# Kernel optimization log

Measured on AMD Instinct MI355X. Metric: run time of the kernel, lower is better.

Reference implementation:

```python
import jax, jax.numpy as jnp
import numpy as np

N_NODES = 50000
N_EDGES = 1600000
F_IN = 128
HID = 128
N_CLS = 16


def setup_inputs() -> dict:
    key = jax.random.key(0)
    ks = jax.random.split(key, 8)
    x = jax.random.normal(ks[0], (N_NODES, F_IN), dtype=jnp.float32)
    edge_index = jax.random.randint(ks[1], (2, N_EDGES), 0, N_NODES, dtype=jnp.int64)
    W1 = jax.random.normal(ks[2], (F_IN, HID), dtype=jnp.float32) * (1.0 / np.sqrt(F_IN))
    b1 = jnp.zeros((HID,), dtype=jnp.float32)
    W2 = jax.random.normal(ks[3], (HID, HID), dtype=jnp.float32) * (1.0 / np.sqrt(HID))
    b2 = jnp.zeros((HID,), dtype=jnp.float32)
    W3 = jax.random.normal(ks[4], (HID, N_CLS), dtype=jnp.float32) * (1.0 / np.sqrt(HID))
    b3 = jnp.zeros((N_CLS,), dtype=jnp.float32)
    return {"x": x, "edge_index": edge_index, "W1": W1, "b1": b1,
            "W2": W2, "b2": b2, "W3": W3, "b3": b3}


def _gcn_norm(edge_index, n_nodes, dtype):
    # PyG gcn_norm with add_self_loops=True, improved=False
    loops = jnp.arange(n_nodes, dtype=edge_index.dtype)
    row = jnp.concatenate([edge_index[0], loops])  # source j
    col = jnp.concatenate([edge_index[1], loops])  # target i
    deg = jax.ops.segment_sum(jnp.ones(row.shape[0], dtype=dtype), col,
                              num_segments=n_nodes)
    dinv = jnp.where(deg > 0, jax.lax.rsqrt(deg), 0.0)
    norm = dinv[row] * dinv[col]  # [E + N]
    return row, col, norm


def _gcn_conv(h, W, b, row, col, norm, n_nodes):
    h = h @ W                              # [N, out] linear first (PyG order)
    msg = h[row] * norm[:, None]           # gather + per-edge scale
    agg = jax.ops.segment_sum(msg, col, num_segments=n_nodes)  # scatter-add
    return agg + b


def reference(x, edge_index, W1, b1, W2, b2, W3, b3):
    n = x.shape[0]
    row, col, norm = _gcn_norm(edge_index, n, x.dtype)
    h = jax.nn.relu(_gcn_conv(x, W1, b1, row, col, norm, n))
    h = jax.nn.relu(_gcn_conv(h, W2, b2, row, col, norm, n))
    h = jax.nn.relu(_gcn_conv(h, W3, b3, row, col, norm, n))
    return h
```

## Files before the change

### kernel.cpp

```cpp
#include <hip/hip_runtime.h>
#include <hip/hip_fp16.h>


static inline int cdiv(int a, int b) { return (a + b - 1) / b; }

__global__ __launch_bounds__(256) void k_zero_int(int* p, int n) {
    int i = blockIdx.x * 256 + threadIdx.x;
    if (i < n) p[i] = 0;
}

__global__ __launch_bounds__(256) void k_count(const int* __restrict__ col, int* cnt, int e) {
    int i = blockIdx.x * 256 + threadIdx.x;
    if (i < e) atomicAdd(&cnt[col[i]], 1);
}

__global__ __launch_bounds__(256) void k_scanA(const int* __restrict__ cnt, int* bsum,
                                               float* __restrict__ dinv, int n) {
    __shared__ int s[256];
    int t = threadIdx.x;
    int i = blockIdx.x * 256 + t;
    int v = (i < n) ? cnt[i] : 0;
    if (i < n) dinv[i] = rsqrtf((float)(v + 1));
    s[t] = v;
    __syncthreads();
    for (int off = 128; off > 0; off >>= 1) {
        if (t < off) s[t] += s[t + off];
        __syncthreads();
    }
    if (t == 0) bsum[blockIdx.x] = s[0];
}

__global__ __launch_bounds__(256) void k_scanB(int* bsum, int nb) {
    __shared__ int s[256];
    int t = threadIdx.x;
    int v = (t < nb) ? bsum[t] : 0;
    s[t] = v;
    for (int off = 1; off < 256; off <<= 1) {
        __syncthreads();
        int x = (t >= off) ? s[t - off] : 0;
        __syncthreads();
        s[t] += x;
    }
    __syncthreads();
    if (t < nb) bsum[t] = s[t] - v;
}

__global__ __launch_bounds__(256) void k_scanC(const int* __restrict__ cnt, const int* __restrict__ bsum,
                                               int* offs, int* cur, int n) {
    __shared__ int s[256];
    int t = threadIdx.x;
    int i = blockIdx.x * 256 + t;
    int v = (i < n) ? cnt[i] : 0;
    s[t] = v;
    for (int off = 1; off < 256; off <<= 1) {
        __syncthreads();
        int x = (t >= off) ? s[t - off] : 0;
        __syncthreads();
        s[t] += x;
    }
    __syncthreads();
    int ov = bsum[blockIdx.x] + s[t] - v;
    if (i <= n) offs[i] = ov;
    if (i < n) cur[i] = ov;
}

__global__ __launch_bounds__(256) void k_fill_xcd(const int* __restrict__ row, const int* __restrict__ col,
                                                  int* cur, unsigned short* __restrict__ csr,
                                                  int e, int n, int nblk) {
    int g = blockIdx.x & 7;
    int b = blockIdx.x >> 3;
    int rs = (n + 7) >> 3;
    int lo = g * rs;
    int hi = min(lo + rs, n);
    int stride = nblk * 256;
    for (int i = b * 256 + threadIdx.x; i < e; i += stride) {
        int c = col[i];
        if (c >= lo && c < hi) {
            int pos = atomicAdd(&cur[c], 1);
            csr[pos] = (unsigned short)row[i];
        }
    }
}

__global__ __launch_bounds__(256) void k_gemm128(const float* __restrict__ X, const float* __restrict__ W,
                                                 const float* __restrict__ dinv,
                                                 __half* __restrict__ Ah, int n) {
    __shared__ float sW[16][128];
    __shared__ float sX[16][128];
    int tid = threadIdx.x;

    int row0 = blockIdx.x * 128;
    int tx = tid & 15, ty = tid >> 4;
    float acc[8][8];
    #pragma unroll
    for (int i = 0; i < 8; ++i)
        #pragma unroll
        for (int j = 0; j < 8; ++j) acc[i][j] = 0.f;

    for (int k0 = 0; k0 < 128; k0 += 16) {
        __syncthreads();
        #pragma unroll
        for (int i = tid; i < 512; i += 256) {
            int kk = i >> 5, c4 = i & 31;
            *(float4*)&sW[kk][c4 * 4] = ((const float4*)W)[(size_t)(k0 + kk) * 32 + c4];
        }
        #pragma unroll
        for (int i = tid; i < 512; i += 256) {
            int r = i >> 2, kq = i & 3;
            int gr = row0 + r;
            float4 v = (gr < n) ? ((const float4*)X)[(size_t)gr * 32 + (k0 >> 2) + kq]
                                : make_float4(0.f, 0.f, 0.f, 0.f);
            sX[kq * 4 + 0][r] = v.x;
            sX[kq * 4 + 1][r] = v.y;
            sX[kq * 4 + 2][r] = v.z;
            sX[kq * 4 + 3][r] = v.w;
        }
        __syncthreads();
        #pragma unroll
        for (int kk = 0; kk < 16; ++kk) {
            float a[8], b[8];
            *(float4*)&a[0] = *(const float4*)&sX[kk][ty * 8];
            *(float4*)&a[4] = *(const float4*)&sX[kk][ty * 8 + 4];
            *(float4*)&b[0] = *(const float4*)&sW[kk][tx * 8];
            *(float4*)&b[4] = *(const float4*)&sW[kk][tx * 8 + 4];
            #pragma unroll
            for (int i = 0; i < 8; ++i)
                #pragma unroll
                for (int j = 0; j < 8; ++j)
                    acc[i][j] = fmaf(a[i], b[j], acc[i][j]);
        }
    }
    #pragma unroll
    for (int i = 0; i < 8; ++i) {
        int gr = row0 + ty * 8 + i;
        if (gr < n) {
            float di = dinv[gr];
            union { uint4 u; __half2 h[4]; } pk;
            pk.h[0] = __floats2half2_rn(di * acc[i][0], di * acc[i][1]);
            pk.h[1] = __floats2half2_rn(di * acc[i][2], di * acc[i][3]);
            pk.h[2] = __floats2half2_rn(di * acc[i][4], di * acc[i][5]);
            pk.h[3] = __floats2half2_rn(di * acc[i][6], di * acc[i][7]);
            ((uint4*)Ah)[(size_t)gr * 16 + tx] = pk.u;
        }
    }
}

__global__ __launch_bounds__(256) void k_gemm16(const float* __restrict__ X, const float* __restrict__ W,
                                                const float* __restrict__ dinv,
                                                __half* __restrict__ Ch, int n) {
    __shared__ float sX[16 * 132];
    __shared__ float sW[128 * 16];
    int tid = threadIdx.x;
    for (int i = tid; i < 512; i += 256)
        ((float4*)sW)[i] = ((const float4*)W)[i];
    int row0 = blockIdx.x * 16;
    for (int i = tid; i < 512; i += 256) {
        int r = i >> 5, c = i & 31;
        int gr = row0 + r;
        float4 v = (gr < n) ? ((const float4*)X)[(size_t)gr * 32 + c]
                            : make_float4(0.f, 0.f, 0.f, 0.f);
        *(float4*)&sX[r * 132 + c * 4] = v;
    }
    __syncthreads();

    int rl = tid >> 4, cj = tid & 15;
    float acc = 0.f;
    #pragma unroll 8
    for (int k = 0; k < 128; ++k)
        acc = fmaf(sX[rl * 132 + k], sW[k * 16 + cj], acc);
    int gr = row0 + rl;
    if (gr < n) Ch[(size_t)gr * 16 + cj] = __float2half_rn(dinv[gr] * acc);
}

__global__ __launch_bounds__(256) void k_agg128(const __half* __restrict__ Hh, const unsigned short* __restrict__ csr,
                                                const int* __restrict__ offs, const float* __restrict__ dinv,
                                                const float* __restrict__ b, float* __restrict__ out, int n) {
    int node = (blockIdx.x * 256 + threadIdx.x) >> 6;
    if (node >= n) return;
    int lane = threadIdx.x & 63;
    int sub  = lane & 31;
    int half = lane >> 5;
    const uint2* H2 = (const uint2*)Hh;
    int ed = offs[node], end = offs[node + 1];
    float4 acc = make_float4(0.f, 0.f, 0.f, 0.f);

    #define EDGE_ADD(R)                                                          \
        {                                                                        \
            uint2 q = H2[(size_t)(R) * 32 + sub];                                \
            float2 f01 = __half22float2(*(const __half2*)&q.x);                  \
            float2 f23 = __half22float2(*(const __half2*)&q.y);                  \
            acc.x += f01.x; acc.y += f01.y;                                      \
            acc.z += f23.x; acc.w += f23.y;                                      \
        }

    for (; ed + 7 < end; ed += 8) {
        int r0 = csr[ed     + half];
        int r1 = csr[ed + 2 + half];
        int r2 = csr[ed + 4 + half];
        int r3 = csr[ed + 6 + half];
        EDGE_ADD(r0); EDGE_ADD(r1); EDGE_ADD(r2); EDGE_ADD(r3);
    }
    #pragma unroll
    for (int s = 0; s < 4; ++s) {
        int idx = ed + 2 * s + half;
        if (idx < end) {
            int r = csr[idx];
            EDGE_ADD(r);
        }
    }
    #undef EDGE_ADD

    acc.x += __shfl_xor(acc.x, 32);
    acc.y += __shfl_xor(acc.y, 32);
    acc.z += __shfl_xor(acc.z, 32);
    acc.w += __shfl_xor(acc.w, 32);

    float di = dinv[node];
    uint2 qh = H2[(size_t)node * 32 + sub];
    float2 h01 = __half22float2(*(const __half2*)&qh.x);
    float2 h23 = __half22float2(*(const __half2*)&qh.y);
    float4 bv = ((const float4*)b)[sub];
    float4 o;
    o.x = fmaxf(fmaf(di, acc.x + h01.x, bv.x), 0.f);
    o.y = fmaxf(fmaf(di, acc.y + h01.y, bv.y), 0.f);
    o.z = fmaxf(fmaf(di, acc.z + h23.x, bv.z), 0.f);
    o.w = fmaxf(fmaf(di, acc.w + h23.y, bv.w), 0.f);
    if (half == 0)
        ((float4*)out)[(size_t)node * 32 + sub] = o;
}

__global__ __launch_bounds__(256) void k_agg16(const __half* __restrict__ Ch, const unsigned short* __restrict__ csr,
                                               const int* __restrict__ offs, const float* __restrict__ dinv,
                                               const float* __restrict__ b, float* __restrict__ out, int n) {
    int t = blockIdx.x * 256 + threadIdx.x;
    int node = t >> 3;
    if (node >= n) return;
    int lane = t & 7;
    int sub  = lane & 3;
    int half = lane >> 2;
    const uint2* C2 = (const uint2*)Ch;
    int ed = offs[node], end = offs[node + 1];
    float4 acc = make_float4(0.f, 0.f, 0.f, 0.f);

    #define EDGE_ADD16(R)                                                        \
        {                                                                        \
            uint2 q = C2[(size_t)(R) * 4 + sub];                                 \
            float2 f01 = __half22float2(*(const __half2*)&q.x);                  \
            float2 f23 = __half22float2(*(const __half2*)&q.y);                  \
            acc.x += f01.x; acc.y += f01.y;                                      \
            acc.z += f23.x; acc.w += f23.y;                                      \
        }

    for (; ed + 3 < end; ed += 4) {
        int r0 = csr[ed     + half];
        int r1 = csr[ed + 2 + half];
        EDGE_ADD16(r0); EDGE_ADD16(r1);
    }
    #pragma unroll
    for (int s = 0; s < 2; ++s) {
        int idx = ed + 2 * s + half;
        if (idx < end) {
            int r = csr[idx];
            EDGE_ADD16(r);
        }
    }
    #undef EDGE_ADD16

    acc.x += __shfl_xor(acc.x, 4);
    acc.y += __shfl_xor(acc.y, 4);
    acc.z += __shfl_xor(acc.z, 4);
    acc.w += __shfl_xor(acc.w, 4);

    float di = dinv[node];
    uint2 qh = C2[(size_t)node * 4 + sub];
    float2 h01 = __half22float2(*(const __half2*)&qh.x);
    float2 h23 = __half22float2(*(const __half2*)&qh.y);
    float4 bv = ((const float4*)b)[sub];
    float4 o;
    o.x = fmaxf(fmaf(di, acc.x + h01.x, bv.x), 0.f);
    o.y = fmaxf(fmaf(di, acc.y + h01.y, bv.y), 0.f);
    o.z = fmaxf(fmaf(di, acc.z + h23.x, bv.z), 0.f);
    o.w = fmaxf(fmaf(di, acc.w + h23.y, bv.w), 0.f);
    if (half == 0)
        ((float4*)out)[(size_t)node * 4 + sub] = o;
}

extern "C" void kernel_launch(void* const* d_in, const int* in_sizes, int n_in,
                              void* d_out, int out_size, void* d_ws, size_t ws_size,
                              hipStream_t stream) {
    const float* x  = (const float*)d_in[0];
    const int*   ei = (const int*)d_in[1];
    const float* W1 = (const float*)d_in[2];
    const float* b1 = (const float*)d_in[3];
    const float* W2 = (const float*)d_in[4];
    const float* b2 = (const float*)d_in[5];
    const float* W3 = (const float*)d_in[6];
    const float* b3 = (const float*)d_in[7];

    const int n = in_sizes[0] / 128;
    const int e = in_sizes[1] / 2;
    const int* row = ei;
    const int* col = ei + e;

    unsigned short* csr = (unsigned short*)d_ws;
    __half* Ah  = (__half*)(csr + ((e + 1) & ~1));
    float*  B   = (float*)(Ah + (size_t)n * 128);
    __half* Ch  = (__half*)(B + (size_t)n * 128);
    float* dinv = (float*)(Ch + (size_t)n * 16);
    int*   offs = (int*)(dinv + n);
    int*   cnt  = offs + (n + 1);
    int*   cur  = cnt + n;
    int*   bsum = cur + n;
    float* out  = (float*)d_out;

    const int nb = cdiv(n + 1, 256);
    const int fillBlocks = 256;

    k_zero_int<<<cdiv(n, 256), 256, 0, stream>>>(cnt, n);
    k_count   <<<cdiv(e, 256), 256, 0, stream>>>(col, cnt, e);
    k_scanA   <<<nb, 256, 0, stream>>>(cnt, bsum, dinv, n);
    k_scanB   <<<1, 256, 0, stream>>>(bsum, nb);
    k_scanC   <<<nb, 256, 0, stream>>>(cnt, bsum, offs, cur, n);
    k_fill_xcd<<<8 * fillBlocks, 256, 0, stream>>>(row, col, cur, csr, e, n, fillBlocks);

    k_gemm128<<<cdiv(n, 128), 256, 0, stream>>>(x, W1, dinv, Ah, n);
    k_agg128 <<<cdiv(n * 64, 256), 256, 0, stream>>>(Ah, csr, offs, dinv, b1, B, n);
    k_gemm128<<<cdiv(n, 128), 256, 0, stream>>>(B, W2, dinv, Ah, n);
    k_agg128 <<<cdiv(n * 64, 256), 256, 0, stream>>>(Ah, csr, offs, dinv, b2, B, n);
    k_gemm16 <<<cdiv(n, 16), 256, 0, stream>>>(B, W3, dinv, Ch, n);
    k_agg16  <<<cdiv(n * 8, 256), 256, 0, stream>>>(Ch, csr, offs, dinv, b3, out, n);
}
```

Before: 353.8 us.

## Vectorize degree count, fold block-sum scan into scanC, unroll aggregation by 16

The degree-count kernel now loads four column indices per thread as an int4 and issues four atomics, cutting thread count and load instructions. The separate single-block scan of block sums is removed; instead each scanC block sums the preceding block totals itself, saving a launch at the cost of redundant reads. The 128-wide aggregation loop gains a 16-edge unrolled stage to keep more gather loads in flight, with added register pressure.

```diff
diff --git a/kernel.cpp b/kernel.cpp
--- a/kernel.cpp
+++ b/kernel.cpp
@@ -9,9 +9,19 @@
     if (i < n) p[i] = 0;
 }
 
-__global__ __launch_bounds__(256) void k_count(const int* __restrict__ col, int* cnt, int e) {
+__global__ __launch_bounds__(256) void k_count4(const int4* __restrict__ col4, int* cnt, int e4,
+                                                const int* __restrict__ col, int e) {
     int i = blockIdx.x * 256 + threadIdx.x;
-    if (i < e) atomicAdd(&cnt[col[i]], 1);
+    if (i < e4) {
+        int4 c = col4[i];
+        atomicAdd(&cnt[c.x], 1);
+        atomicAdd(&cnt[c.y], 1);
+        atomicAdd(&cnt[c.z], 1);
+        atomicAdd(&cnt[c.w], 1);
+    }
+    if (i == 0) {
+        for (int k = e4 * 4; k < e; ++k) atomicAdd(&cnt[col[k]], 1);
+    }
 }
 
 __global__ __launch_bounds__(256) void k_scanA(const int* __restrict__ cnt, int* bsum,
@@ -30,25 +40,20 @@
     if (t == 0) bsum[blockIdx.x] = s[0];
 }
 
-__global__ __launch_bounds__(256) void k_scanB(int* bsum, int nb) {
-    __shared__ int s[256];
-    int t = threadIdx.x;
-    int v = (t < nb) ? bsum[t] : 0;
-    s[t] = v;
-    for (int off = 1; off < 256; off <<= 1) {
-        __syncthreads();
-        int x = (t >= off) ? s[t - off] : 0;
-        __syncthreads();
-        s[t] += x;
-    }
-    __syncthreads();
-    if (t < nb) bsum[t] = s[t] - v;
-}
-
 __global__ __launch_bounds__(256) void k_scanC(const int* __restrict__ cnt, const int* __restrict__ bsum,
                                                int* offs, int* cur, int n) {
     __shared__ int s[256];
     int t = threadIdx.x;
+    int p = 0;
+    for (int j = t; j < (int)blockIdx.x; j += 256) p += bsum[j];
+    s[t] = p;
+    __syncthreads();
+    for (int off = 128; off > 0; off >>= 1) {
+        if (t < off) s[t] += s[t + off];
+        __syncthreads();
+    }
+    int blockPrefix = s[0];
+    __syncthreads();
     int i = blockIdx.x * 256 + t;
     int v = (i < n) ? cnt[i] : 0;
     s[t] = v;
@@ -59,7 +64,7 @@
         s[t] += x;
     }
     __syncthreads();
-    int ov = bsum[blockIdx.x] + s[t] - v;
+    int ov = blockPrefix + s[t] - v;
     if (i <= n) offs[i] = ov;
     if (i < n) cur[i] = ov;
 }
@@ -193,6 +198,18 @@
             acc.z += f23.x; acc.w += f23.y;                                      \
         }
 
+    for (; ed + 15 < end; ed += 16) {
+        int r0 = csr[ed      + half];
+        int r1 = csr[ed + 2  + half];
+        int r2 = csr[ed + 4  + half];
+        int r3 = csr[ed + 6  + half];
+        int r4 = csr[ed + 8  + half];
+        int r5 = csr[ed + 10 + half];
+        int r6 = csr[ed + 12 + half];
+        int r7 = csr[ed + 14 + half];
+        EDGE_ADD(r0); EDGE_ADD(r1); EDGE_ADD(r2); EDGE_ADD(r3);
+        EDGE_ADD(r4); EDGE_ADD(r5); EDGE_ADD(r6); EDGE_ADD(r7);
+    }
     for (; ed + 7 < end; ed += 8) {
         int r0 = csr[ed     + half];
         int r1 = csr[ed + 2 + half];
@@ -314,12 +331,12 @@
     float* out  = (float*)d_out;
 
     const int nb = cdiv(n + 1, 256);
+    const int e4 = e >> 2;
     const int fillBlocks = 256;
 
     k_zero_int<<<cdiv(n, 256), 256, 0, stream>>>(cnt, n);
-    k_count   <<<cdiv(e, 256), 256, 0, stream>>>(col, cnt, e);
+    k_count4  <<<cdiv(e4, 256), 256, 0, stream>>>((const int4*)col, cnt, e4, col, e);
     k_scanA   <<<nb, 256, 0, stream>>>(cnt, bsum, dinv, n);
-    k_scanB   <<<1, 256, 0, stream>>>(bsum, nb);
     k_scanC   <<<nb, 256, 0, stream>>>(cnt, bsum, offs, cur, n);
     k_fill_xcd<<<8 * fillBlocks, 256, 0, stream>>>(row, col, cur, csr, e, n, fillBlocks);
 
```

Result: no change. 348.6 us (-1.5%).
